# Performance work log

Hardware: AMD Instinct MI355X
Metric: run time of the kernel (lower is better)

## Reference

```python
import jax, jax.numpy as jnp
import numpy as np

TH = 1.0            # q_threshold for all IF neurons
POS_MAX = 7.0       # level//2 - 1, level=16, sym=True
NEG_MIN = -8.0      # -(level//2)
PREFIRE = 0.2       # attn_softmax_IF.prefire
S_QUANT = 7.0       # spiking_softmax scale = level//2 - 1
NUM_HEADS = 8


def if_step(x, vmem0, acc0, th=TH, pos_max=POS_MAX, neg_min=NEG_MIN):
    """One timestep of a symmetric ST-BIF neuron with straight-through surrogate.
    Forward: spike in {-1,0,+1}*th gated by membrane and accumulator saturation.
    Backward: identity (STE), accumulator is a constant."""
    acc0f = acc0.astype(x.dtype)
    v = vmem0 + x
    pos = jnp.logical_and(v >= th, acc0f < pos_max)
    neg = jnp.logical_and(v < 0.0, acc0f > neg_min)
    spike = pos.astype(x.dtype) - neg.astype(x.dtype)
    out_hard = spike * th
    out = x + jax.lax.stop_gradient(out_hard - x)  # STE: fwd=spike*th, bwd=identity
    acc = jax.lax.stop_gradient(acc0f + spike)     # running spike count (constant wrt grads)
    return out, acc


def setup_inputs() -> dict:
    key = jax.random.key(0)
    ks = jax.random.split(key, 16)
    B, N, C, H = 4, 1024, 512, NUM_HEADS
    D = C // H
    f32 = jnp.float32
    inp = {
        "x": jax.random.normal(ks[0], (B, N, C), dtype=f32),
        "w_qkv": jax.random.normal(ks[1], (3 * C, C), dtype=f32) * 0.02,
        "b_qkv": jnp.zeros((3 * C,), dtype=f32),
        "w_proj": jax.random.normal(ks[2], (C, C), dtype=f32) * 0.02,
        "b_proj": jnp.zeros((C,), dtype=f32),
        "q_vmem": jax.random.uniform(ks[3], (B, H, N, D), dtype=f32),
        "k_vmem": jax.random.uniform(ks[4], (B, H, N, D), dtype=f32),
        "v_vmem": jax.random.uniform(ks[5], (B, H, N, D), dtype=f32),
        "attn_vmem": jax.random.uniform(ks[6], (B, H, N, N), dtype=f32),
        "q_acc0": jax.random.randint(ks[7], (B, H, N, D), 0, 8).astype(jnp.int32),
        "k_acc0": jax.random.randint(ks[8], (B, H, N, D), 0, 8).astype(jnp.int32),
        "v_acc0": jax.random.randint(ks[9], (B, H, N, D), 0, 8).astype(jnp.int32),
        "attn_acc0": jax.random.randint(ks[10], (B, H, N, N), 0, 8).astype(jnp.int32),
    }
    return inp


def reference(x, w_qkv, b_qkv, w_proj, b_proj,
              q_vmem, k_vmem, v_vmem, attn_vmem,
              q_acc0, k_acc0, v_acc0, attn_acc0):
    B, N, C = x.shape
    H = NUM_HEADS
    D = C // H
    scale = D ** -0.5
    sg = jax.lax.stop_gradient

    # qkv projection -> [3, B, H, N, D]
    qkv = (x @ w_qkv.T + b_qkv).reshape(B, N, 3, H, D).transpose(2, 0, 3, 1, 4)
    q_in, k_in, v_in = qkv[0], qkv[1], qkv[2]

    # ST-BIF IF neurons (one timestep, carried state)
    q_s, q_acc = if_step(q_in, q_vmem, q_acc0)
    k_s, k_acc = if_step(k_in, k_vmem, k_acc0)
    v_s, v_acc = if_step(v_in, v_vmem, v_acc0)

    q = q_s * scale
    # accumulator corrections: acc_q * q_threshold (*scale for q) minus detached spike output
    q_corr = sg(q_acc * TH * scale - q)
    k_corr = sg(k_acc * TH - k_s)
    v_corr = sg(v_acc * TH - v_s)

    # multi: (q + q_corr) @ k^T + q @ k_corr^T   -> [B, H, N, N]
    attn = (jnp.einsum('bhnd,bhmd->bhnm', q + q_corr, k_s)
            + jnp.einsum('bhnd,bhmd->bhnm', q, k_corr))

    # spiking softmax substitute: softmax of the (accumulated) scores, scaled to quant range
    attn = jax.nn.softmax(attn, axis=-1) * S_QUANT

    # attn_softmax_IF with prefire bias on the membrane
    attn_s, attn_acc = if_step(attn, attn_vmem + PREFIRE * TH, attn_acc0)
    attn_corr = sg(attn_acc * TH - attn_s)

    # multi1: (attn + attn_corr) @ v + attn @ v_corr  -> [B, H, N, D]
    out = (jnp.einsum('bhnm,bhmd->bhnd', attn_s + attn_corr, v_s)
           + jnp.einsum('bhnm,bhmd->bhnd', attn_s, v_corr))

    # after_attn_IF: fresh state (rounding init 0.5*th, zero accumulator)
    out, _ = if_step(out, jnp.asarray(0.5 * TH, out.dtype), jnp.zeros_like(out))

    out = out.transpose(0, 2, 1, 3).reshape(B, N, C)
    return out @ w_proj.T + b_proj
```

## Files before the change

### kernel.cpp

```cpp
#include <hip/hip_runtime.h>
#include <hip/hip_bf16.h>

typedef short short8 __attribute__((ext_vector_type(8)));
typedef float f32x4 __attribute__((ext_vector_type(4)));

using bf16 = __hip_bfloat16;

#define MFMA16(a, b, c) __builtin_amdgcn_mfma_f32_16x16x32_bf16((a), (b), (c), 0, 0, 0)

__device__ __forceinline__ short8 ldb8(const bf16* p) {
    return *reinterpret_cast<const short8*>(p);
}
__device__ __forceinline__ unsigned int bfu(float f) {
    union { float f; unsigned int u; } x{f};
    return x.u >> 16;
}

__global__ __launch_bounds__(256) void k_cast(const float* __restrict__ src,
                                              bf16* __restrict__ dst, int n)
{
    for (int i = blockIdx.x * 256 + threadIdx.x; i < n; i += gridDim.x * 256)
        dst[i] = __float2bfloat16(src[i]);
}

__global__ __launch_bounds__(256, 3) void k_qkv_f32(
    const float* __restrict__ X, const float* __restrict__ W, const float* __restrict__ bq,
    const float* __restrict__ qvm, const float* __restrict__ kvm, const float* __restrict__ vvm,
    const int* __restrict__ qac, const int* __restrict__ kac, const int* __restrict__ vac,
    bf16* __restrict__ Q2, bf16* __restrict__ K2c, bf16* __restrict__ VsT, bf16* __restrict__ VaT)
{
    __shared__ float As[16][64];
    __shared__ float Bs[16][128];
    const int tid = threadIdx.x;
    const int r0 = blockIdx.y * 64;
    const int c0 = blockIdx.x * 128;
    const int tm = (tid & 15) * 4;
    const int tn = (tid >> 4) * 8;
    const int arow = tid >> 2, ak = (tid & 3) * 4;
    const int brow = tid >> 1, bk = (tid & 1) * 8;

    float acc[4][8] = {};
    for (int kk = 0; kk < 512; kk += 16) {
        const float4 a4 = *reinterpret_cast<const float4*>(X + (size_t)(r0 + arow) * 512 + kk + ak);
        const float4 w0 = *reinterpret_cast<const float4*>(W + (size_t)(c0 + brow) * 512 + kk + bk);
        const float4 w1 = *reinterpret_cast<const float4*>(W + (size_t)(c0 + brow) * 512 + kk + bk + 4);
        __syncthreads();
        As[ak + 0][arow] = a4.x; As[ak + 1][arow] = a4.y; As[ak + 2][arow] = a4.z; As[ak + 3][arow] = a4.w;
        Bs[bk + 0][brow] = w0.x; Bs[bk + 1][brow] = w0.y; Bs[bk + 2][brow] = w0.z; Bs[bk + 3][brow] = w0.w;
        Bs[bk + 4][brow] = w1.x; Bs[bk + 5][brow] = w1.y; Bs[bk + 6][brow] = w1.z; Bs[bk + 7][brow] = w1.w;
        __syncthreads();
        #pragma unroll
        for (int k = 0; k < 16; ++k) {
            const float4 av = *reinterpret_cast<const float4*>(&As[k][tm]);
            const float4 bv0 = *reinterpret_cast<const float4*>(&Bs[k][tn]);
            const float4 bv1 = *reinterpret_cast<const float4*>(&Bs[k][tn + 4]);
            const float ar[4] = {av.x, av.y, av.z, av.w};
            const float br[8] = {bv0.x, bv0.y, bv0.z, bv0.w, bv1.x, bv1.y, bv1.z, bv1.w};
            #pragma unroll
            for (int i = 0; i < 4; ++i)
                #pragma unroll
                for (int j = 0; j < 8; ++j)
                    acc[i][j] += ar[i] * br[j];
        }
    }

    const int sel = c0 >> 9;
    const int h   = ((c0 + tn) & 511) >> 6;
    const int d0  = (c0 + tn) & 63;
    const float4 bb0 = *reinterpret_cast<const float4*>(bq + c0 + tn);
    const float4 bb1 = *reinterpret_cast<const float4*>(bq + c0 + tn + 4);
    const float bcol[8] = {bb0.x, bb0.y, bb0.z, bb0.w, bb1.x, bb1.y, bb1.z, bb1.w};

    const float* VM = (sel == 0) ? qvm : (sel == 1) ? kvm : vvm;
    const int*   AC = (sel == 0) ? qac : (sel == 1) ? kac : vac;
    float vmv[4][8]; int acv[4][8]; int bhn[4];
    #pragma unroll
    for (int i = 0; i < 4; ++i) {
        const int r = r0 + tm + i;
        const int b = r >> 10, n = r & 1023;
        const int bh = b * 8 + h;
        bhn[i] = bh * 1024 + n;
        const size_t i4 = (size_t)bhn[i] * 64 + d0;
        const float4 v0 = *reinterpret_cast<const float4*>(VM + i4);
        const float4 v1 = *reinterpret_cast<const float4*>(VM + i4 + 4);
        const int4  c0i = *reinterpret_cast<const int4*>(AC + i4);
        const int4  c1i = *reinterpret_cast<const int4*>(AC + i4 + 4);
        vmv[i][0]=v0.x; vmv[i][1]=v0.y; vmv[i][2]=v0.z; vmv[i][3]=v0.w;
        vmv[i][4]=v1.x; vmv[i][5]=v1.y; vmv[i][6]=v1.z; vmv[i][7]=v1.w;
        acv[i][0]=c0i.x; acv[i][1]=c0i.y; acv[i][2]=c0i.z; acv[i][3]=c0i.w;
        acv[i][4]=c1i.x; acv[i][5]=c1i.y; acv[i][6]=c1i.z; acv[i][7]=c1i.w;
    }

    int spm[4][8];
    #pragma unroll
    for (int i = 0; i < 4; ++i)
        #pragma unroll
        for (int j = 0; j < 8; ++j) {
            const float v_ = vmv[i][j] + (acc[i][j] + bcol[j]);
            int sp = ((v_ >= 1.0f) && (acv[i][j] < 7)) ? 1 : 0;
            if (v_ < 0.0f) sp -= 1;
            spm[i][j] = sp;
        }

    if (sel == 2) {
        #pragma unroll
        for (int j = 0; j < 8; ++j) {
            const int nb = (r0 & 1023) + tm;
            uint2 us, ua;
            us.x = bfu((float)spm[0][j]) | (bfu((float)spm[1][j]) << 16);
            us.y = bfu((float)spm[2][j]) | (bfu((float)spm[3][j]) << 16);
            ua.x = bfu((float)acv[0][j]) | (bfu((float)acv[1][j]) << 16);
            ua.y = bfu((float)acv[2][j]) | (bfu((float)acv[3][j]) << 16);
            const size_t vi = ((size_t)((bhn[0] >> 10) * 64 + d0 + j)) * 1024 + nb;
            *reinterpret_cast<uint2*>(VsT + vi) = us;
            *reinterpret_cast<uint2*>(VaT + vi) = ua;
        }
    } else {
        #pragma unroll
        for (int i = 0; i < 4; ++i) {
            uint4 p0, p1;
            unsigned u0[8], u1[8];
            #pragma unroll
            for (int j = 0; j < 8; ++j) {
                if (sel == 0) { u0[j] = bfu((float)(acv[i][j] + spm[i][j])); u1[j] = bfu((float)spm[i][j]); }
                else          { u0[j] = bfu((float)spm[i][j]);               u1[j] = bfu((float)acv[i][j]); }
            }
            p0.x = u0[0]|(u0[1]<<16); p0.y = u0[2]|(u0[3]<<16); p0.z = u0[4]|(u0[5]<<16); p0.w = u0[6]|(u0[7]<<16);
            p1.x = u1[0]|(u1[1]<<16); p1.y = u1[2]|(u1[3]<<16); p1.z = u1[4]|(u1[5]<<16); p1.w = u1[6]|(u1[7]<<16);
            bf16* base = ((sel == 0) ? Q2 : K2c) + (size_t)bhn[i] * 128 + d0;
            *reinterpret_cast<uint4*>(base)      = p0;
            *reinterpret_cast<uint4*>(base + 64) = p1;
        }
    }
}

__global__ __launch_bounds__(256, 2) void k_attn(
    const bf16* __restrict__ Q2, const bf16* __restrict__ K2c,
    const float* __restrict__ avm, const int* __restrict__ aac,
    const bf16* __restrict__ VsT, const bf16* __restrict__ VaT,
    bf16* __restrict__ O2)
{
    __shared__ float S[16 * 1024];
    char* const Sc = (char*)S;
    const int w = threadIdx.x >> 6, lane = threadIdx.x & 63;
    const int lo = lane & 15, hi = lane >> 4;
    const int h = blockIdx.y, bb = blockIdx.z;
    const int bh = bb * 8 + h;
    const int n0 = blockIdx.x * 16;

    {
        const bf16* qb = Q2 + ((size_t)(bh * 1024 + n0 + lo)) * 128 + hi * 8;
        const short8 a0 = ldb8(qb), a1 = ldb8(qb + 32), a2 = ldb8(qb + 64), a3 = ldb8(qb + 96);
        const bf16* kbp = K2c + ((size_t)(bh * 1024 + w * 256 + lo)) * 128 + hi * 8;
        short8 b0 = ldb8(kbp), b1 = ldb8(kbp + 32), b2 = ldb8(kbp + 64), b3 = ldb8(kbp + 96);
        for (int t = 0; t < 16; ++t) {
            const short8 c0f = b0, c1f = b1, c2f = b2, c3f = b3;
            if (t < 15) {
                kbp += 16 * 128;
                b0 = ldb8(kbp); b1 = ldb8(kbp + 32); b2 = ldb8(kbp + 64); b3 = ldb8(kbp + 96);
            }
            f32x4 acc = {0.f, 0.f, 0.f, 0.f};
            acc = MFMA16(a0, c0f, acc);
            acc = MFMA16(a1, c1f, acc);
            acc = MFMA16(a2, c2f, acc);
            acc = MFMA16(a3, c3f, acc);
            const int cc = w * 256 + t * 16 + lo;
            const int sbase = ((cc >> 9) << 13) + (cc & 511);
            #pragma unroll
            for (int r = 0; r < 4; ++r)
                S[sbase + (hi * 4 + r) * 512] = 0.125f * acc[r];
        }
    }

    const int row = threadIdx.x >> 4, q = threadIdx.x & 15;
    const size_t gRow = ((size_t)bh * 1024 + (n0 + row)) * 1024;
    float4 vmv[16]; int4 acv[16];
    #pragma unroll
    for (int j = 0; j < 8; ++j) {
        const int cb = (q + 16 * j) * 8;
        vmv[2*j]   = *reinterpret_cast<const float4*>(avm + gRow + cb);
        vmv[2*j+1] = *reinterpret_cast<const float4*>(avm + gRow + cb + 4);
        acv[2*j]   = *reinterpret_cast<const int4*>(aac + gRow + cb);
        acv[2*j+1] = *reinterpret_cast<const int4*>(aac + gRow + cb + 4);
    }
    __syncthreads();

    float mx = -3.0e38f;
    #pragma unroll 8
    for (int j = 0; j < 64; ++j) {
        const int c = q + (j << 4);
        mx = fmaxf(mx, S[((c >> 9) << 13) + row * 512 + (c & 511)]);
    }
    mx = fmaxf(mx, __shfl_xor(mx, 1));
    mx = fmaxf(mx, __shfl_xor(mx, 2));
    mx = fmaxf(mx, __shfl_xor(mx, 4));
    mx = fmaxf(mx, __shfl_xor(mx, 8));
    float sum = 0.f;
    #pragma unroll 8
    for (int j = 0; j < 64; ++j) {
        const int c = q + (j << 4);
        const int si = ((c >> 9) << 13) + row * 512 + (c & 511);
        const float e = expf(S[si] - mx);
        S[si] = e;
        sum += e;
    }
    sum += __shfl_xor(sum, 1);
    sum += __shfl_xor(sum, 2);
    sum += __shfl_xor(sum, 4);
    sum += __shfl_xor(sum, 8);
    __syncthreads();

    float4 eA[8];
    #pragma unroll
    for (int j = 0; j < 4; ++j) {
        const int cb = (q + 16 * j) * 8;
        eA[2*j]   = *reinterpret_cast<const float4*>(&S[row * 512 + cb]);
        eA[2*j+1] = *reinterpret_cast<const float4*>(&S[row * 512 + cb + 4]);
    }
    __syncthreads();

    #pragma unroll
    for (int j = 0; j < 4; ++j) {
        const int kb = q + 16 * j;
        const float ev[8] = {eA[2*j].x, eA[2*j].y, eA[2*j].z, eA[2*j].w,
                             eA[2*j+1].x, eA[2*j+1].y, eA[2*j+1].z, eA[2*j+1].w};
        const float vmr[8] = {vmv[2*j].x, vmv[2*j].y, vmv[2*j].z, vmv[2*j].w,
                              vmv[2*j+1].x, vmv[2*j+1].y, vmv[2*j+1].z, vmv[2*j+1].w};
        const int aar[8] = {acv[2*j].x, acv[2*j].y, acv[2*j].z, acv[2*j].w,
                            acv[2*j+1].x, acv[2*j+1].y, acv[2*j+1].z, acv[2*j+1].w};
        unsigned p1u[8], p2u[8];
        #pragma unroll
        for (int i = 0; i < 8; ++i) {
            const float p7 = (ev[i] / sum) * 7.0f;
            const float v_ = (vmr[i] + 0.2f) + p7;
            const int a0i = aar[i];
            const int sp = ((v_ >= 1.0f) && (a0i < 7)) ? 1 : 0;
            p1u[i] = bfu((float)(a0i + sp));
            p2u[i] = bfu((float)sp);
        }
        uint4 w1, w2;
        w1.x = p1u[0]|(p1u[1]<<16); w1.y = p1u[2]|(p1u[3]<<16); w1.z = p1u[4]|(p1u[5]<<16); w1.w = p1u[6]|(p1u[7]<<16);
        w2.x = p2u[0]|(p2u[1]<<16); w2.y = p2u[2]|(p2u[3]<<16); w2.z = p2u[4]|(p2u[5]<<16); w2.w = p2u[6]|(p2u[7]<<16);
        char* pb = Sc + row * 2048 + ((kb ^ row) & 63) * 16;
        *reinterpret_cast<uint4*>(pb)        = w1;
        *reinterpret_cast<uint4*>(pb + 1024) = w2;
    }

    float4 eB[8];
    #pragma unroll
    for (int j = 4; j < 8; ++j) {
        const int cb = (q + 16 * j) * 8;
        eB[2*(j-4)]   = *reinterpret_cast<const float4*>(&S[8192 + row * 512 + (cb - 512)]);
        eB[2*(j-4)+1] = *reinterpret_cast<const float4*>(&S[8192 + row * 512 + (cb - 512) + 4]);
    }
    __syncthreads();

    #pragma unroll
    for (int j = 4; j < 8; ++j) {
        const int kb = q + 16 * j;
        const int jj = j - 4;
        const float ev[8] = {eB[2*jj].x, eB[2*jj].y, eB[2*jj].z, eB[2*jj].w,
                             eB[2*jj+1].x, eB[2*jj+1].y, eB[2*jj+1].z, eB[2*jj+1].w};
        const float vmr[8] = {vmv[2*j].x, vmv[2*j].y, vmv[2*j].z, vmv[2*j].w,
                              vmv[2*j+1].x, vmv[2*j+1].y, vmv[2*j+1].z, vmv[2*j+1].w};
        const int aar[8] = {acv[2*j].x, acv[2*j].y, acv[2*j].z, acv[2*j].w,
                            acv[2*j+1].x, acv[2*j+1].y, acv[2*j+1].z, acv[2*j+1].w};
        unsigned p1u[8], p2u[8];
        #pragma unroll
        for (int i = 0; i < 8; ++i) {
            const float p7 = (ev[i] / sum) * 7.0f;
            const float v_ = (vmr[i] + 0.2f) + p7;
            const int a0i = aar[i];
            const int sp = ((v_ >= 1.0f) && (a0i < 7)) ? 1 : 0;
            p1u[i] = bfu((float)(a0i + sp));
            p2u[i] = bfu((float)sp);
        }
        uint4 w1, w2;
        w1.x = p1u[0]|(p1u[1]<<16); w1.y = p1u[2]|(p1u[3]<<16); w1.z = p1u[4]|(p1u[5]<<16); w1.w = p1u[6]|(p1u[7]<<16);
        w2.x = p2u[0]|(p2u[1]<<16); w2.y = p2u[2]|(p2u[3]<<16); w2.z = p2u[4]|(p2u[5]<<16); w2.w = p2u[6]|(p2u[7]<<16);
        char* pb = Sc + 32768 + row * 2048 + ((kb & 63) ^ row) * 16;
        *reinterpret_cast<uint4*>(pb)        = w1;
        *reinterpret_cast<uint4*>(pb + 1024) = w2;
    }
    __syncthreads();

    {
        const int d0 = w * 16;
        const bf16* vs = VsT + ((size_t)(bh * 64 + d0 + lo)) * 1024 + hi * 8;
        const bf16* va = VaT + ((size_t)(bh * 64 + d0 + lo)) * 1024 + hi * 8;
        short8 nvs = ldb8(vs), nva = ldb8(va);
        f32x4 acc = {0.f, 0.f, 0.f, 0.f};
        for (int tt = 0; tt < 32; ++tt) {
            const short8 cvs = nvs, cva = nva;
            if (tt < 31) { nvs = ldb8(vs + (tt + 1) * 32); nva = ldb8(va + (tt + 1) * 32); }
            const int kb_lin = tt * 4 + hi;
            const char* pb = Sc + (kb_lin >> 6) * 32768 + lo * 2048 + (((kb_lin & 63) ^ lo)) * 16;
            const short8 a1 = *reinterpret_cast<const short8*>(pb);
            const short8 a2 = *reinterpret_cast<const short8*>(pb + 1024);
            acc = MFMA16(a1, cvs, acc);
            acc = MFMA16(a2, cva, acc);
        }
        #pragma unroll
        for (int r = 0; r < 4; ++r) {
            const int n = n0 + hi * 4 + r;
            const float o = acc[r];
            const float o2 = (o >= 0.5f ? 1.f : 0.f) - (o < -0.5f ? 1.f : 0.f);
            O2[((size_t)(bb * 1024 + n)) * 512 + h * 64 + d0 + lo] = __float2bfloat16(o2);
        }
    }
}

__global__ __launch_bounds__(256) void k_proj(
    const bf16* __restrict__ O2, const bf16* __restrict__ W, const float* __restrict__ bias,
    float* __restrict__ Y)
{
    const int w = threadIdx.x >> 6, lane = threadIdx.x & 63;
    const int lo = lane & 15, hi = lane >> 4;
    const int r0 = blockIdx.y * 16;
    const int c0 = blockIdx.x * 256 + w * 64;

    f32x4 acc[4] = {{0.f,0.f,0.f,0.f},{0.f,0.f,0.f,0.f},{0.f,0.f,0.f,0.f},{0.f,0.f,0.f,0.f}};
    const bf16* op = O2 + (size_t)(r0 + lo) * 512 + hi * 8;
    #pragma unroll 4
    for (int kb = 0; kb < 16; ++kb) {
        short8 a = ldb8(op + kb * 32);
        #pragma unroll
        for (int t = 0; t < 4; ++t) {
            short8 b = ldb8(W + (size_t)(c0 + t * 16 + lo) * 512 + kb * 32 + hi * 8);
            acc[t] = MFMA16(a, b, acc[t]);
        }
    }
    #pragma unroll
    for (int t = 0; t < 4; ++t) {
        const int col = c0 + t * 16 + lo;
        const float bcol = bias[col];
        #pragma unroll
        for (int r = 0; r < 4; ++r) {
            const int rr = r0 + hi * 4 + r;
            Y[(size_t)rr * 512 + col] = acc[t][r] + bcol;
        }
    }
}

extern "C" void kernel_launch(void* const* d_in, const int* in_sizes, int n_in,
                              void* d_out, int out_size, void* d_ws, size_t ws_size,
                              hipStream_t stream)
{
    const float* x     = (const float*)d_in[0];
    const float* wqkv  = (const float*)d_in[1];
    const float* bqkv  = (const float*)d_in[2];
    const float* wproj = (const float*)d_in[3];
    const float* bproj = (const float*)d_in[4];
    const float* qvm   = (const float*)d_in[5];
    const float* kvm   = (const float*)d_in[6];
    const float* vvm   = (const float*)d_in[7];
    const float* avm   = (const float*)d_in[8];
    const int*   qac   = (const int*)d_in[9];
    const int*   kac   = (const int*)d_in[10];
    const int*   vac   = (const int*)d_in[11];
    const int*   aac   = (const int*)d_in[12];

    char* p = (char*)d_ws;
    bf16* Q2  = (bf16*)p; p += (size_t)32 * 1024 * 128 * 2;
    bf16* K2c = (bf16*)p; p += (size_t)32 * 1024 * 128 * 2;
    bf16* VsT = (bf16*)p; p += (size_t)32 * 64 * 1024 * 2;
    bf16* VaT = (bf16*)p; p += (size_t)32 * 64 * 1024 * 2;
    bf16* O2  = (bf16*)p; p += (size_t)4096 * 512 * 2;
    bf16* Wp  = (bf16*)p; p += (size_t)512 * 512 * 2;

    k_cast<<<dim3(256), 256, 0, stream>>>(wproj, Wp, 512 * 512);
    k_qkv_f32<<<dim3(12, 64), 256, 0, stream>>>(x, wqkv, bqkv, qvm, kvm, vvm,
                                                qac, kac, vac, Q2, K2c, VsT, VaT);
    k_attn<<<dim3(64, 8, 4), 256, 0, stream>>>(Q2, K2c, avm, aac, VsT, VaT, O2);
    k_proj<<<dim3(2, 256), 256, 0, stream>>>(O2, Wp, bproj, (float*)d_out);
}
```

Baseline: 527.1 us.

## Switch attention operands to int8 MFMA and keep scores as int16 in LDS

Stores Q/K/V spike and accumulator tensors as int8 instead of bf16 and runs both attention matmuls with i32 16x16x64 int8 MFMA. Raw scores go to LDS as int16, which halves shared memory and allows four blocks per CU instead of two. The softmax now works from register-held scores, recomputing exp in the final pass instead of writing it back to LDS. Membrane and accumulator loads are software-pipelined across a three-slot register rotation. The values are small integers, so int8 is exact, but the LDS swizzle layout and register pressure change.

After: 511.6 us. 2.9% less time.

```diff
diff --git a/kernel.cpp b/kernel.cpp
--- a/kernel.cpp
+++ b/kernel.cpp
@@ -1,19 +1,21 @@
 #include <hip/hip_runtime.h>
 #include <hip/hip_bf16.h>
+#include <cstdint>
 
 typedef short short8 __attribute__((ext_vector_type(8)));
 typedef float f32x4 __attribute__((ext_vector_type(4)));
+typedef int   int4v __attribute__((ext_vector_type(4)));
 
 using bf16 = __hip_bfloat16;
 
 #define MFMA16(a, b, c) __builtin_amdgcn_mfma_f32_16x16x32_bf16((a), (b), (c), 0, 0, 0)
+#define MFMAI8(a, b, c) __builtin_amdgcn_mfma_i32_16x16x64_i8((a), (b), (c), 0, 0, 0)
 
 __device__ __forceinline__ short8 ldb8(const bf16* p) {
     return *reinterpret_cast<const short8*>(p);
 }
-__device__ __forceinline__ unsigned int bfu(float f) {
-    union { float f; unsigned int u; } x{f};
-    return x.u >> 16;
+__device__ __forceinline__ unsigned pk4(int a, int b, int c, int d) {
+    return (a & 255) | ((b & 255) << 8) | ((c & 255) << 16) | ((d & 255) << 24);
 }
 
 __global__ __launch_bounds__(256) void k_cast(const float* __restrict__ src,
@@ -27,7 +29,7 @@
     const float* __restrict__ X, const float* __restrict__ W, const float* __restrict__ bq,
     const float* __restrict__ qvm, const float* __restrict__ kvm, const float* __restrict__ vvm,
     const int* __restrict__ qac, const int* __restrict__ kac, const int* __restrict__ vac,
-    bf16* __restrict__ Q2, bf16* __restrict__ K2c, bf16* __restrict__ VsT, bf16* __restrict__ VaT)
+    int8_t* __restrict__ Q2, int8_t* __restrict__ K2c, int8_t* __restrict__ VsT, int8_t* __restrict__ VaT)
 {
     __shared__ float As[16][64];
     __shared__ float Bs[16][128];
@@ -106,42 +108,39 @@
         #pragma unroll
         for (int j = 0; j < 8; ++j) {
             const int nb = (r0 & 1023) + tm;
-            uint2 us, ua;
-            us.x = bfu((float)spm[0][j]) | (bfu((float)spm[1][j]) << 16);
-            us.y = bfu((float)spm[2][j]) | (bfu((float)spm[3][j]) << 16);
-            ua.x = bfu((float)acv[0][j]) | (bfu((float)acv[1][j]) << 16);
-            ua.y = bfu((float)acv[2][j]) | (bfu((float)acv[3][j]) << 16);
+            const unsigned us = pk4(spm[0][j], spm[1][j], spm[2][j], spm[3][j]);
+            const unsigned ua = pk4(acv[0][j], acv[1][j], acv[2][j], acv[3][j]);
             const size_t vi = ((size_t)((bhn[0] >> 10) * 64 + d0 + j)) * 1024 + nb;
-            *reinterpret_cast<uint2*>(VsT + vi) = us;
-            *reinterpret_cast<uint2*>(VaT + vi) = ua;
+            *reinterpret_cast<unsigned*>(VsT + vi) = us;
+            *reinterpret_cast<unsigned*>(VaT + vi) = ua;
         }
     } else {
         #pragma unroll
         for (int i = 0; i < 4; ++i) {
-            uint4 p0, p1;
-            unsigned u0[8], u1[8];
+            int v0[8], v1[8];
             #pragma unroll
             for (int j = 0; j < 8; ++j) {
-                if (sel == 0) { u0[j] = bfu((float)(acv[i][j] + spm[i][j])); u1[j] = bfu((float)spm[i][j]); }
-                else          { u0[j] = bfu((float)spm[i][j]);               u1[j] = bfu((float)acv[i][j]); }
+                if (sel == 0) { v0[j] = acv[i][j] + spm[i][j]; v1[j] = spm[i][j]; }
+                else          { v0[j] = spm[i][j];             v1[j] = acv[i][j]; }
             }
-            p0.x = u0[0]|(u0[1]<<16); p0.y = u0[2]|(u0[3]<<16); p0.z = u0[4]|(u0[5]<<16); p0.w = u0[6]|(u0[7]<<16);
-            p1.x = u1[0]|(u1[1]<<16); p1.y = u1[2]|(u1[3]<<16); p1.z = u1[4]|(u1[5]<<16); p1.w = u1[6]|(u1[7]<<16);
-            bf16* base = ((sel == 0) ? Q2 : K2c) + (size_t)bhn[i] * 128 + d0;
-            *reinterpret_cast<uint4*>(base)      = p0;
-            *reinterpret_cast<uint4*>(base + 64) = p1;
-        }
-    }
-}
-
-__global__ __launch_bounds__(256, 2) void k_attn(
-    const bf16* __restrict__ Q2, const bf16* __restrict__ K2c,
+            uint2 a, b;
+            a.x = pk4(v0[0], v0[1], v0[2], v0[3]); a.y = pk4(v0[4], v0[5], v0[6], v0[7]);
+            b.x = pk4(v1[0], v1[1], v1[2], v1[3]); b.y = pk4(v1[4], v1[5], v1[6], v1[7]);
+            int8_t* base = ((sel == 0) ? Q2 : K2c) + (size_t)bhn[i] * 128 + d0;
+            *reinterpret_cast<uint2*>(base)      = a;
+            *reinterpret_cast<uint2*>(base + 64) = b;
+        }
+    }
+}
+
+__global__ __launch_bounds__(256, 4) void k_attn(
+    const int8_t* __restrict__ Q2, const int8_t* __restrict__ K2c,
     const float* __restrict__ avm, const int* __restrict__ aac,
-    const bf16* __restrict__ VsT, const bf16* __restrict__ VaT,
+    const int8_t* __restrict__ VsT, const int8_t* __restrict__ VaT,
     bf16* __restrict__ O2)
 {
-    __shared__ float S[16 * 1024];
-    char* const Sc = (char*)S;
+    __shared__ alignas(16) char Sc[32768];
+    short* const Ss = (short*)Sc;
     const int w = threadIdx.x >> 6, lane = threadIdx.x & 63;
     const int lo = lane & 15, hi = lane >> 4;
     const int h = blockIdx.y, bb = blockIdx.z;
@@ -149,165 +148,152 @@
     const int n0 = blockIdx.x * 16;
 
     {
-        const bf16* qb = Q2 + ((size_t)(bh * 1024 + n0 + lo)) * 128 + hi * 8;
-        const short8 a0 = ldb8(qb), a1 = ldb8(qb + 32), a2 = ldb8(qb + 64), a3 = ldb8(qb + 96);
-        const bf16* kbp = K2c + ((size_t)(bh * 1024 + w * 256 + lo)) * 128 + hi * 8;
-        short8 b0 = ldb8(kbp), b1 = ldb8(kbp + 32), b2 = ldb8(kbp + 64), b3 = ldb8(kbp + 96);
+        const int8_t* qb = Q2 + ((size_t)(bh * 1024 + n0 + lo)) * 128 + hi * 16;
+        const int4v a0 = *reinterpret_cast<const int4v*>(qb);
+        const int4v a1 = *reinterpret_cast<const int4v*>(qb + 64);
+        const int8_t* kbp = K2c + ((size_t)(bh * 1024 + w * 256 + lo)) * 128 + hi * 16;
+        int4v b0 = *reinterpret_cast<const int4v*>(kbp);
+        int4v b1 = *reinterpret_cast<const int4v*>(kbp + 64);
         for (int t = 0; t < 16; ++t) {
-            const short8 c0f = b0, c1f = b1, c2f = b2, c3f = b3;
+            const int4v c0f = b0, c1f = b1;
             if (t < 15) {
                 kbp += 16 * 128;
-                b0 = ldb8(kbp); b1 = ldb8(kbp + 32); b2 = ldb8(kbp + 64); b3 = ldb8(kbp + 96);
+                b0 = *reinterpret_cast<const int4v*>(kbp);
+                b1 = *reinterpret_cast<const int4v*>(kbp + 64);
             }
-            f32x4 acc = {0.f, 0.f, 0.f, 0.f};
-            acc = MFMA16(a0, c0f, acc);
-            acc = MFMA16(a1, c1f, acc);
-            acc = MFMA16(a2, c2f, acc);
-            acc = MFMA16(a3, c3f, acc);
+            int4v acc = {0, 0, 0, 0};
+            acc = MFMAI8(a0, c0f, acc);
+            acc = MFMAI8(a1, c1f, acc);
             const int cc = w * 256 + t * 16 + lo;
-            const int sbase = ((cc >> 9) << 13) + (cc & 511);
+            short* sb = Ss + ((cc >> 9) << 13) + (cc & 511);
             #pragma unroll
             for (int r = 0; r < 4; ++r)
-                S[sbase + (hi * 4 + r) * 512] = 0.125f * acc[r];
+                sb[(hi * 4 + r) << 9] = (short)acc[r];
         }
     }
 
     const int row = threadIdx.x >> 4, q = threadIdx.x & 15;
     const size_t gRow = ((size_t)bh * 1024 + (n0 + row)) * 1024;
-    float4 vmv[16]; int4 acv[16];
+
+#define LOADJ(j, VM0, VM1, AC0, AC1) {                                          \
+        const int cb_ = (q + 16 * (j)) * 8;                                     \
+        VM0 = *reinterpret_cast<const float4*>(avm + gRow + cb_);               \
+        VM1 = *reinterpret_cast<const float4*>(avm + gRow + cb_ + 4);           \
+        AC0 = *reinterpret_cast<const int4*>(aac + gRow + cb_);                 \
+        AC1 = *reinterpret_cast<const int4*>(aac + gRow + cb_ + 4); }
+
+    float4 vmA0, vmA1, vmB0, vmB1, vmC0, vmC1;
+    int4   acA0, acA1, acB0, acB1, acC0, acC1;
+    LOADJ(0, vmA0, vmA1, acA0, acA1);
+    LOADJ(1, vmB0, vmB1, acB0, acB1);
+
+    __syncthreads();
+
+    short8 sc[8];
     #pragma unroll
     for (int j = 0; j < 8; ++j) {
-        const int cb = (q + 16 * j) * 8;
-        vmv[2*j]   = *reinterpret_cast<const float4*>(avm + gRow + cb);
-        vmv[2*j+1] = *reinterpret_cast<const float4*>(avm + gRow + cb + 4);
-        acv[2*j]   = *reinterpret_cast<const int4*>(aac + gRow + cb);
-        acv[2*j+1] = *reinterpret_cast<const int4*>(aac + gRow + cb + 4);
+        const int kb = q + 16 * j;
+        sc[j] = *reinterpret_cast<const short8*>(Sc + ((kb >> 6) << 14) + (row << 10) + ((kb & 63) << 4));
     }
     __syncthreads();
 
-    float mx = -3.0e38f;
-    #pragma unroll 8
-    for (int j = 0; j < 64; ++j) {
-        const int c = q + (j << 4);
-        mx = fmaxf(mx, S[((c >> 9) << 13) + row * 512 + (c & 511)]);
-    }
+    LOADJ(2, vmC0, vmC1, acC0, acC1);
+
+    int mxi = sc[0][0];
+    #pragma unroll
+    for (int j = 0; j < 8; ++j)
+        #pragma unroll
+        for (int i = 0; i < 8; ++i)
+            mxi = max(mxi, (int)sc[j][i]);
+    float mx = 0.125f * (float)mxi;
     mx = fmaxf(mx, __shfl_xor(mx, 1));
     mx = fmaxf(mx, __shfl_xor(mx, 2));
     mx = fmaxf(mx, __shfl_xor(mx, 4));
     mx = fmaxf(mx, __shfl_xor(mx, 8));
+
     float sum = 0.f;
-    #pragma unroll 8
-    for (int j = 0; j < 64; ++j) {
-        const int c = q + (j << 4);
-        const int si = ((c >> 9) << 13) + row * 512 + (c & 511);
-        const float e = expf(S[si] - mx);
-        S[si] = e;
-        sum += e;
-    }
+    #pragma unroll
+    for (int j = 0; j < 8; ++j)
+        #pragma unroll
+        for (int i = 0; i < 8; ++i)
+            sum += expf(0.125f * (float)sc[j][i] - mx);
     sum += __shfl_xor(sum, 1);
     sum += __shfl_xor(sum, 2);
     sum += __shfl_xor(sum, 4);
     sum += __shfl_xor(sum, 8);
-    __syncthreads();
-
-    float4 eA[8];
-    #pragma unroll
-    for (int j = 0; j < 4; ++j) {
-        const int cb = (q + 16 * j) * 8;
-        eA[2*j]   = *reinterpret_cast<const float4*>(&S[row * 512 + cb]);
-        eA[2*j+1] = *reinterpret_cast<const float4*>(&S[row * 512 + cb + 4]);
-    }
-    __syncthreads();
-
-    #pragma unroll
-    for (int j = 0; j < 4; ++j) {
-        const int kb = q + 16 * j;
-        const float ev[8] = {eA[2*j].x, eA[2*j].y, eA[2*j].z, eA[2*j].w,
-                             eA[2*j+1].x, eA[2*j+1].y, eA[2*j+1].z, eA[2*j+1].w};
-        const float vmr[8] = {vmv[2*j].x, vmv[2*j].y, vmv[2*j].z, vmv[2*j].w,
-                              vmv[2*j+1].x, vmv[2*j+1].y, vmv[2*j+1].z, vmv[2*j+1].w};
-        const int aar[8] = {acv[2*j].x, acv[2*j].y, acv[2*j].z, acv[2*j].w,
-                            acv[2*j+1].x, acv[2*j+1].y, acv[2*j+1].z, acv[2*j+1].w};
-        unsigned p1u[8], p2u[8];
-        #pragma unroll
-        for (int i = 0; i < 8; ++i) {
-            const float p7 = (ev[i] / sum) * 7.0f;
-            const float v_ = (vmr[i] + 0.2f) + p7;
-            const int a0i = aar[i];
-            const int sp = ((v_ >= 1.0f) && (a0i < 7)) ? 1 : 0;
-            p1u[i] = bfu((float)(a0i + sp));
-            p2u[i] = bfu((float)sp);
-        }
-        uint4 w1, w2;
-        w1.x = p1u[0]|(p1u[1]<<16); w1.y = p1u[2]|(p1u[3]<<16); w1.z = p1u[4]|(p1u[5]<<16); w1.w = p1u[6]|(p1u[7]<<16);
-        w2.x = p2u[0]|(p2u[1]<<16); w2.y = p2u[2]|(p2u[3]<<16); w2.z = p2u[4]|(p2u[5]<<16); w2.w = p2u[6]|(p2u[7]<<16);
-        char* pb = Sc + row * 2048 + ((kb ^ row) & 63) * 16;
-        *reinterpret_cast<uint4*>(pb)        = w1;
-        *reinterpret_cast<uint4*>(pb + 1024) = w2;
-    }
-
-    float4 eB[8];
-    #pragma unroll
-    for (int j = 4; j < 8; ++j) {
-        const int cb = (q + 16 * j) * 8;
-        eB[2*(j-4)]   = *reinterpret_cast<const float4*>(&S[8192 + row * 512 + (cb - 512)]);
-        eB[2*(j-4)+1] = *reinterpret_cast<const float4*>(&S[8192 + row * 512 + (cb - 512) + 4]);
-    }
-    __syncthreads();
-
-    #pragma unroll
-    for (int j = 4; j < 8; ++j) {
-        const int kb = q + 16 * j;
-        const int jj = j - 4;
-        const float ev[8] = {eB[2*jj].x, eB[2*jj].y, eB[2*jj].z, eB[2*jj].w,
-                             eB[2*jj+1].x, eB[2*jj+1].y, eB[2*jj+1].z, eB[2*jj+1].w};
-        const float vmr[8] = {vmv[2*j].x, vmv[2*j].y, vmv[2*j].z, vmv[2*j].w,
-                              vmv[2*j+1].x, vmv[2*j+1].y, vmv[2*j+1].z, vmv[2*j+1].w};
-        const int aar[8] = {acv[2*j].x, acv[2*j].y, acv[2*j].z, acv[2*j].w,
-                            acv[2*j+1].x, acv[2*j+1].y, acv[2*j+1].z, acv[2*j+1].w};
-        unsigned p1u[8], p2u[8];
-        #pragma unroll
-        for (int i = 0; i < 8; ++i) {
-            const float p7 = (ev[i] / sum) * 7.0f;
-            const float v_ = (vmr[i] + 0.2f) + p7;
-            const int a0i = aar[i];
-            const int sp = ((v_ >= 1.0f) && (a0i < 7)) ? 1 : 0;
-            p1u[i] = bfu((float)(a0i + sp));
-            p2u[i] = bfu((float)sp);
-        }
-        uint4 w1, w2;
-        w1.x = p1u[0]|(p1u[1]<<16); w1.y = p1u[2]|(p1u[3]<<16); w1.z = p1u[4]|(p1u[5]<<16); w1.w = p1u[6]|(p1u[7]<<16);
-        w2.x = p2u[0]|(p2u[1]<<16); w2.y = p2u[2]|(p2u[3]<<16); w2.z = p2u[4]|(p2u[5]<<16); w2.w = p2u[6]|(p2u[7]<<16);
-        char* pb = Sc + 32768 + row * 2048 + ((kb & 63) ^ row) * 16;
-        *reinterpret_cast<uint4*>(pb)        = w1;
-        *reinterpret_cast<uint4*>(pb + 1024) = w2;
-    }
+
+#define PSTEP(j, VM0, VM1, AC0, AC1) {                                          \
+        const float vmr_[8] = {VM0.x, VM0.y, VM0.z, VM0.w,                      \
+                               VM1.x, VM1.y, VM1.z, VM1.w};                     \
+        const int aar_[8] = {AC0.x, AC0.y, AC0.z, AC0.w,                        \
+                             AC1.x, AC1.y, AC1.z, AC1.w};                       \
+        unsigned p1u[8], p2u[8];                                                \
+        _Pragma("unroll")                                                       \
+        for (int i = 0; i < 8; ++i) {                                           \
+            const float e_ = expf(0.125f * (float)sc[j][i] - mx);               \
+            const float p7 = (e_ / sum) * 7.0f;                                 \
+            const float v_ = (vmr_[i] + 0.2f) + p7;          \
+            const int a0i = aar_[i];                              \
+            const int sp = ((v_ >= 1.0f) && (a0i < 7)) ? 1 : 0;                 \
+            p1u[i] = (unsigned)(a0i + sp);                                      \
+            p2u[i] = (unsigned)sp;                                              \
+        }                                                                       \
+        uint2 w1, w2;                                                           \
+        w1.x = p1u[0] | (p1u[1] << 8) | (p1u[2] << 16) | (p1u[3] << 24);        \
+        w1.y = p1u[4] | (p1u[5] << 8) | (p1u[6] << 16) | (p1u[7] << 24);        \
+        w2.x = p2u[0] | (p2u[1] << 8) | (p2u[2] << 16) | (p2u[3] << 24);        \
+        w2.y = p2u[4] | (p2u[5] << 8) | (p2u[6] << 16) | (p2u[7] << 24);        \
+        const int kb = q + 16 * (j);                                            \
+        char* pb = Sc + (row << 10) + (((kb << 3) ^ ((row & 7) << 4)));         \
+        *reinterpret_cast<uint2*>(pb)         = w1;                             \
+        *reinterpret_cast<uint2*>(pb + 16384) = w2; }
+
+    PSTEP(0, vmA0, vmA1, acA0, acA1);
+    LOADJ(3, vmA0, vmA1, acA0, acA1);
+    PSTEP(1, vmB0, vmB1, acB0, acB1);
+    LOADJ(4, vmB0, vmB1, acB0, acB1);
+    PSTEP(2, vmC0, vmC1, acC0, acC1);
+    LOADJ(5, vmC0, vmC1, acC0, acC1);
+    PSTEP(3, vmA0, vmA1, acA0, acA1);
+    LOADJ(6, vmA0, vmA1, acA0, acA1);
+    PSTEP(4, vmB0, vmB1, acB0, acB1);
+    LOADJ(7, vmB0, vmB1, acB0, acB1);
+    PSTEP(5, vmC0, vmC1, acC0, acC1);
+    PSTEP(6, vmA0, vmA1, acA0, acA1);
+    PSTEP(7, vmB0, vmB1, acB0, acB1);
+
     __syncthreads();
 
     {
         const int d0 = w * 16;
-        const bf16* vs = VsT + ((size_t)(bh * 64 + d0 + lo)) * 1024 + hi * 8;
-        const bf16* va = VaT + ((size_t)(bh * 64 + d0 + lo)) * 1024 + hi * 8;
-        short8 nvs = ldb8(vs), nva = ldb8(va);
-        f32x4 acc = {0.f, 0.f, 0.f, 0.f};
-        for (int tt = 0; tt < 32; ++tt) {
-            const short8 cvs = nvs, cva = nva;
-            if (tt < 31) { nvs = ldb8(vs + (tt + 1) * 32); nva = ldb8(va + (tt + 1) * 32); }
-            const int kb_lin = tt * 4 + hi;
-            const char* pb = Sc + (kb_lin >> 6) * 32768 + lo * 2048 + (((kb_lin & 63) ^ lo)) * 16;
-            const short8 a1 = *reinterpret_cast<const short8*>(pb);
-            const short8 a2 = *reinterpret_cast<const short8*>(pb + 1024);
-            acc = MFMA16(a1, cvs, acc);
-            acc = MFMA16(a2, cva, acc);
+        const int8_t* vs = VsT + ((size_t)(bh * 64 + d0 + lo)) * 1024 + hi * 16;
+        const int8_t* va = VaT + ((size_t)(bh * 64 + d0 + lo)) * 1024 + hi * 16;
+        int4v nvs = *reinterpret_cast<const int4v*>(vs);
+        int4v nva = *reinterpret_cast<const int4v*>(va);
+        int4v acc = {0, 0, 0, 0};
+        for (int tt = 0; tt < 16; ++tt) {
+            const int4v cvs = nvs, cva = nva;
+            if (tt < 15) {
+                nvs = *reinterpret_cast<const int4v*>(vs + (tt + 1) * 64);
+                nva = *reinterpret_cast<const int4v*>(va + (tt + 1) * 64);
+            }
+            const int off = (tt * 64 + hi * 16) ^ ((lo & 7) << 4);
+            const char* pb = Sc + (lo << 10) + off;
+            const int4v a1 = *reinterpret_cast<const int4v*>(pb);
+            const int4v a2 = *reinterpret_cast<const int4v*>(pb + 16384);
+            acc = MFMAI8(a1, cvs, acc);
+            acc = MFMAI8(a2, cva, acc);
         }
         #pragma unroll
         for (int r = 0; r < 4; ++r) {
             const int n = n0 + hi * 4 + r;
-            const float o = acc[r];
+            const float o = (float)acc[r];
             const float o2 = (o >= 0.5f ? 1.f : 0.f) - (o < -0.5f ? 1.f : 0.f);
             O2[((size_t)(bb * 1024 + n)) * 512 + h * 64 + d0 + lo] = __float2bfloat16(o2);
         }
     }
+#undef LOADJ
+#undef PSTEP
 }
 
 __global__ __launch_bounds__(256) void k_proj(
@@ -361,12 +347,12 @@
     const int*   aac   = (const int*)d_in[12];
 
     char* p = (char*)d_ws;
-    bf16* Q2  = (bf16*)p; p += (size_t)32 * 1024 * 128 * 2;
-    bf16* K2c = (bf16*)p; p += (size_t)32 * 1024 * 128 * 2;
-    bf16* VsT = (bf16*)p; p += (size_t)32 * 64 * 1024 * 2;
-    bf16* VaT = (bf16*)p; p += (size_t)32 * 64 * 1024 * 2;
-    bf16* O2  = (bf16*)p; p += (size_t)4096 * 512 * 2;
-    bf16* Wp  = (bf16*)p; p += (size_t)512 * 512 * 2;
+    int8_t* Q2  = (int8_t*)p; p += (size_t)32 * 1024 * 128;
+    int8_t* K2c = (int8_t*)p; p += (size_t)32 * 1024 * 128;
+    int8_t* VsT = (int8_t*)p; p += (size_t)32 * 64 * 1024;
+    int8_t* VaT = (int8_t*)p; p += (size_t)32 * 64 * 1024;
+    bf16*   O2  = (bf16*)p;   p += (size_t)4096 * 512 * 2;
+    bf16*   Wp  = (bf16*)p;   p += (size_t)512 * 512 * 2;
 
     k_cast<<<dim3(256), 256, 0, stream>>>(wproj, Wp, 512 * 512);
     k_qkv_f32<<<dim3(12, 64), 256, 0, stream>>>(x, wqkv, bqkv, qvm, kvm, vvm,
```
